# Kernel tuning notes

Hardware: AMD Instinct MI355X
Metric: run time of the kernel (lower is better)

Reference implementation:

```python
import jax, jax.numpy as jnp
import numpy as np

NBUS = 33
B33 = [(1,2),(2,3),(3,4),(4,5),(5,6),(6,7),(7,8),(8,9),(9,10),(10,11),(11,12),(12,13),(13,14),(14,15),(15,16),(16,17),(17,18),(2,19),(19,20),(20,21),(21,22),(3,23),(23,24),(24,25),(6,26),(26,27),(27,28),(28,29),(29,30),(30,31),(31,32),(32,33)]


def setup_inputs() -> dict:
    key = jax.random.key(0)
    k1, k2, k3 = jax.random.split(key, 3)
    B, W, M, F = 32, 128, 100, 8
    N, H, GH, K = NBUS, 256, 128, 3
    rng = np.random.default_rng(0)
    br = np.array(B33) - 1
    src = np.concatenate([br[:, 0], br[:, 1]])
    dst = np.concatenate([br[:, 1], br[:, 0]])
    w_half = rng.uniform(0.5, 2.0, size=br.shape[0]).astype(np.float32)
    p = lambda *s: jnp.asarray(rng.normal(0.0, 0.02, size=s).astype(np.float32))
    z = lambda *s: jnp.zeros(s, jnp.float32)
    return {
        'r_seq': jax.random.normal(k1, (B, W, M), jnp.float32),
        'feat_seq': jax.random.normal(k2, (B, W, F), jnp.float32),
        'x_wls_seq': jax.random.normal(k3, (B, W, 2 * N), jnp.float32),
        'edge_index': jnp.asarray(np.stack([src, dst]).astype(np.int32)),
        'edge_weight': jnp.asarray(np.concatenate([w_half, w_half])),
        'pre_w': p(F + 2, GH), 'pre_b': z(GH),
        'tag_w1': p(K + 1, GH, GH), 'tag_b1': z(GH),
        'tag_w2': p(K + 1, GH, GH), 'tag_b2': z(GH),
        'post_w': p(GH, H), 'post_b': z(H),
        'tp_w1': p(M + 2 * N, H), 'tp_b1': z(H),
        'tp_w2': p(H, H), 'tp_b2': z(H),
        'gru_wih0': p(H, 3 * H), 'gru_whh0': p(H, 3 * H), 'gru_bih0': z(3 * H), 'gru_bhh0': z(3 * H),
        'gru_wih1': p(H, 3 * H), 'gru_whh1': p(H, 3 * H), 'gru_bih1': z(3 * H), 'gru_bhh1': z(3 * H),
        'fg_w': p(H, H), 'fg_b': z(H),
        'fs_w': p(H, H), 'fs_b': z(H),
        'gate_w': p(2 * H, H), 'gate_b': z(H),
        'd1_w': p(H, H), 'd1_b': z(H),
        'd2_w': p(H, 2), 'd2_b': z(2),
    }


def _gru_layer(x, wih, whh, bih, bhh):
    # x: (B, W, Din); torch GRU gate order [r, z, n]
    def step(h, xt):
        gi = xt @ wih + bih
        gh = h @ whh + bhh
        ir, iz, inn = jnp.split(gi, 3, axis=-1)
        hr, hz, hn = jnp.split(gh, 3, axis=-1)
        r = jax.nn.sigmoid(ir + hr)
        zt = jax.nn.sigmoid(iz + hz)
        n = jnp.tanh(inn + r * hn)
        h = (1.0 - zt) * n + zt * h
        return h, h
    h0 = jnp.zeros((x.shape[0], whh.shape[0]), x.dtype)
    _, ys = jax.lax.scan(step, h0, jnp.swapaxes(x, 0, 1))
    return jnp.swapaxes(ys, 0, 1)


def _forward(r_seq, feat_seq, x_wls_seq, edge_index, edge_weight,
             pre_w, pre_b, tag_w1, tag_b1, tag_w2, tag_b2, post_w, post_b,
             tp_w1, tp_b1, tp_w2, tp_b2,
             gru_wih0, gru_whh0, gru_bih0, gru_bhh0,
             gru_wih1, gru_whh1, gru_bih1, gru_bhh1,
             fg_w, fg_b, fs_w, fs_b, gate_w, gate_b,
             d1_w, d1_b, d2_w, d2_b):
    B, W, M = r_seq.shape
    N = NBUS
    # ---- spatial branch (batched TAGConv, K=3, 2 layers) ----
    va = x_wls_seq[..., :N, None]
    vm = x_wls_seq[..., N:, None]
    x_nodes = jnp.concatenate([va, vm], axis=-1)                 # (B,W,N,2)
    feat_n = jnp.broadcast_to(feat_seq[:, :, None, :], (B, W, N, feat_seq.shape[-1]))
    gin = jnp.concatenate([feat_n, x_nodes], axis=-1) @ pre_w + pre_b  # (B,W,N,GH)
    g = gin.reshape(B * W, N, gin.shape[-1])
    src, dst = edge_index[0], edge_index[1]
    # gcn_norm (no self-loops), shared across all B*W graph copies
    deg = jnp.zeros((N,), g.dtype).at[dst].add(edge_weight)
    dinv = jnp.where(deg > 0, deg ** -0.5, 0.0)
    norm = dinv[src] * edge_weight * dinv[dst]                   # (E,)

    def prop(h):  # out[i] = sum_{j->i} norm * h[j], batched over graphs
        return jnp.zeros_like(h).at[:, dst].add(h[:, src] * norm[None, :, None])

    def tag(h, Wk, b):  # TAGConv: sum_k A^k h @ W_k + b
        out = h @ Wk[0]
        hk = h
        for k in range(1, Wk.shape[0]):
            hk = prop(hk)
            out = out + hk @ Wk[k]
        return out + b

    g = jax.nn.relu(tag(g, tag_w1, tag_b1))
    g = tag(g, tag_w2, tag_b2)
    g = g.reshape(B, W, N, -1) @ post_w + post_b                 # (B,W,N,H)
    # ---- temporal branch (MLP -> 2-layer GRU); E_time=None skips MHA ----
    s = jnp.concatenate([r_seq, x_wls_seq], axis=-1)
    s = jax.nn.relu(s @ tp_w1 + tp_b1)
    s = jax.nn.relu(s @ tp_w2 + tp_b2)
    s = _gru_layer(s, gru_wih0, gru_whh0, gru_bih0, gru_bhh0)
    s = _gru_layer(s, gru_wih1, gru_whh1, gru_bih1, gru_bhh1)    # (B,W,H)
    # ---- gated fusion + decoder ----
    g_t = g @ fg_w + fg_b                                        # (B,W,N,H)
    s_t = (s @ fs_w + fs_b)[:, :, None, :]                       # (B,W,1,H)
    s_full = jnp.broadcast_to(s_t, g_t.shape)
    alpha = jax.nn.sigmoid(jnp.concatenate([g_t, s_full], axis=-1) @ gate_w + gate_b)
    u = alpha * g_t + (1.0 - alpha) * s_full
    u = jax.nn.relu(u @ d1_w + d1_b) @ d2_w + d2_b               # (B,W,N,2)
    dx = jnp.concatenate([u[..., 0], u[..., 1]], axis=-1)        # (B,W,2N)
    return x_wls_seq + dx


def reference(r_seq, feat_seq, x_wls_seq, edge_index, edge_weight,
              pre_w, pre_b, tag_w1, tag_b1, tag_w2, tag_b2, post_w, post_b,
              tp_w1, tp_b1, tp_w2, tp_b2,
              gru_wih0, gru_whh0, gru_bih0, gru_bhh0,
              gru_wih1, gru_whh1, gru_bih1, gru_bhh1,
              fg_w, fg_b, fs_w, fs_b, gate_w, gate_b,
              d1_w, d1_b, d2_w, d2_b):
    return _forward(r_seq, feat_seq, x_wls_seq, edge_index, edge_weight,
                    pre_w, pre_b, tag_w1, tag_b1, tag_w2, tag_b2, post_w, post_b,
                    tp_w1, tp_b1, tp_w2, tp_b2,
                    gru_wih0, gru_whh0, gru_bih0, gru_bhh0,
                    gru_wih1, gru_whh1, gru_bih1, gru_bhh1,
                    fg_w, fg_b, fs_w, fs_b, gate_w, gate_b,
                    d1_w, d1_b, d2_w, d2_b)
```

## Files before the change

### kernel.cpp

```cpp
#include <hip/hip_runtime.h>
#include <hip/hip_fp16.h>
#include <cmath>

#define DEV __device__ __forceinline__

typedef unsigned short ushortT;
typedef short bs8 __attribute__((ext_vector_type(8)));
typedef float f32x4 __attribute__((ext_vector_type(4)));
typedef _Float16 f16x2 __attribute__((ext_vector_type(2)));

constexpr int kBW = 4096;
constexpr int kM = 100, kF = 8, kN = 33, kH = 256, kGH = 128, kE = 64;

constexpr int OFF_ROWPTR  = 0;
constexpr int OFF_COLSRC  = 64;
constexpr int OFF_COLNORM = 128;
constexpr int OFF_C       = 192;
constexpr int OFF_WC      = 512;
constexpr int OFF_SPRE    = 33280;
constexpr int OFF_GI      = OFF_SPRE + kBW * kH;
constexpr int OFF_SFUSE   = OFF_GI + kBW * 3 * kH;
constexpr int OFF_SGATE   = OFF_SFUSE + kBW * kH;
constexpr int OFF_WQ0     = OFF_SFUSE;
constexpr int OFF_WQ1     = OFF_SFUSE + 98304;
constexpr int WB_TW1  = 0;
constexpr int WB_TW2  = 65536;
constexpr int WB_WC   = 131072;
constexpr int WB_GATE = 163840;
constexpr int WB_D1   = 229376;
constexpr int WB_TOT  = 294912;

DEV float frcp(float x) { return __builtin_amdgcn_rcpf(x); }
DEV float fsig(float x) { return frcp(1.0f + __expf(-x)); }
DEV float ftanh(float x) { float e = __expf(2.0f * x); return 1.0f - 2.0f * frcp(e + 1.0f); }

DEV ushortT f2bf(float x) {
  unsigned u = __float_as_uint(x);
  unsigned r = u + 0x7fffu + ((u >> 16) & 1u);
  return (ushortT)(r >> 16);
}
DEV float bf2f(ushortT u) { return __uint_as_float(((unsigned)u) << 16); }

DEV f32x4 mfma16(bs8 a, bs8 b, f32x4 c) {
  return __builtin_amdgcn_mfma_f32_16x16x32_bf16(a, b, c, 0, 0, 0);
}
DEV bs8 ldb(const ushortT* p) { return *reinterpret_cast<const bs8*>(p); }

#if __has_builtin(__builtin_amdgcn_fdot2)
DEV float dot2(unsigned w, unsigned hp, float acc) {
  f16x2 wv = __builtin_bit_cast(f16x2, w);
  f16x2 hv = __builtin_bit_cast(f16x2, hp);
  return __builtin_amdgcn_fdot2(wv, hv, acc, false);
}
#else
DEV float dot2(unsigned w, unsigned hp, float acc) {
  f16x2 wv = __builtin_bit_cast(f16x2, w);
  f16x2 hv = __builtin_bit_cast(f16x2, hp);
  acc = fmaf((float)wv.x, (float)hv.x, acc);
  acc = fmaf((float)wv.y, (float)hv.y, acc);
  return acc;
}
#endif

__global__ void k_prep(const int* __restrict__ ei, const float* __restrict__ ew,
                       float* __restrict__ ws) {
  if (blockIdx.x != 0 || threadIdx.x != 0) return;
  int* rowptr = (int*)(ws + OFF_ROWPTR);
  int* colsrc = (int*)(ws + OFF_COLSRC);
  float* colnorm = ws + OFF_COLNORM;
  const int* src = ei;
  const int* dst = ei + kE;
  float deg[kN]; int cnt[kN];
  for (int n = 0; n < kN; ++n) { deg[n] = 0.f; cnt[n] = 0; }
  for (int e = 0; e < kE; ++e) { deg[dst[e]] += ew[e]; cnt[dst[e]]++; }
  float dinv[kN];
  for (int n = 0; n < kN; ++n) dinv[n] = deg[n] > 0.f ? 1.0f / sqrtf(deg[n]) : 0.f;
  int pos[kN];
  int run = 0;
  for (int n = 0; n < kN; ++n) { rowptr[n] = run; pos[n] = run; run += cnt[n]; }
  rowptr[kN] = run;
  for (int e = 0; e < kE; ++e) {
    int d = dst[e];
    int p = pos[d]++;
    colsrc[p] = src[e];
    colnorm[p] = dinv[src[e]] * ew[e] * dinv[d];
  }
}

__global__ void k_wcfold(const float* __restrict__ post_w, const float* __restrict__ post_b,
                         const float* __restrict__ fg_w, const float* __restrict__ fg_b,
                         float* __restrict__ ws) {
  const int j = threadIdx.x;
  if ((int)blockIdx.x < kGH) {
    const int k = blockIdx.x;
    float a = 0.f;
    #pragma unroll 4
    for (int m = 0; m < kH; ++m) a = fmaf(post_w[k * kH + m], fg_w[m * kH + j], a);
    ws[OFF_WC + k * kH + j] = a;
  } else {
    float a = fg_b[j];
    #pragma unroll 4
    for (int m = 0; m < kH; ++m) a = fmaf(post_b[m], fg_w[m * kH + j], a);
    ws[OFF_C + j] = a;
  }
}

__global__ void k_wq(const float* __restrict__ w0, const float* __restrict__ w1,
                     float* __restrict__ ws) {
  const int idx = blockIdx.x * 256 + threadIdx.x;
  if (idx >= 2 * 98304) return;
  const int layer = idx / 98304;
  const int rem = idx - layer * 98304;
  const int p = rem / 768, j = rem - p * 768;
  const float* w = layer ? w1 : w0;
  unsigned* dst = (unsigned*)(ws + (layer ? OFF_WQ1 : OFF_WQ0));
  __half2 v = __floats2half2_rn(w[(2 * p) * 768 + j], w[(2 * p + 1) * 768 + j]);
  dst[rem] = *reinterpret_cast<unsigned*>(&v);
}

__global__ void k_wprep(const float* __restrict__ tw1, const float* __restrict__ tw2,
                        const float* __restrict__ gatew, const float* __restrict__ d1w,
                        float* __restrict__ ws) {
  const int idx = blockIdx.x * 256 + threadIdx.x;
  if (idx >= WB_TOT) return;
  ushortT* WB = (ushortT*)(ws + OFF_GI);
  float v; int dst;
  if (idx < 65536) {
    int s = idx >> 14, r = idx & 16383, k = r >> 7, col = r & 127;
    v = tw1[(s << 14) + (k << 7) + col]; dst = WB_TW1 + (s << 14) + (col << 7) + k;
  } else if (idx < 131072) {
    int i = idx - 65536; int s = i >> 14, r = i & 16383, k = r >> 7, col = r & 127;
    v = tw2[(s << 14) + (k << 7) + col]; dst = WB_TW2 + (s << 14) + (col << 7) + k;
  } else if (idx < 163840) {
    int i = idx - 131072; int k = i & 127, col = i >> 7;
    v = ws[OFF_WC + (k << 8) + col]; dst = WB_WC + (col << 7) + k;
  } else if (idx < 229376) {
    int i = idx - 163840; int k = i & 255, col = i >> 8;
    v = gatew[(k << 8) + col]; dst = WB_GATE + (col << 8) + k;
  } else {
    int i = idx - 229376; int k = i & 255, col = i >> 8;
    v = d1w[(k << 8) + col]; dst = WB_D1 + (col << 8) + k;
  }
  WB[dst] = f2bf(v);
}

__global__ __launch_bounds__(256) void k_tpmlp(
    const float* __restrict__ r_seq, const float* __restrict__ x_wls,
    const float* __restrict__ w1, const float* __restrict__ b1,
    const float* __restrict__ w2, const float* __restrict__ b2,
    float* __restrict__ sout) {
  __shared__ float inr[16][kM + 2 * kN];
  __shared__ float h1[16][kH];
  const int bw0 = blockIdx.x * 16, tid = threadIdx.x;
  #pragma unroll
  for (int r = 0; r < 16; ++r) {
    for (int c = tid; c < kM + 2 * kN; c += 256)
      inr[r][c] = (c < kM) ? r_seq[(bw0 + r) * kM + c]
                           : x_wls[(bw0 + r) * 2 * kN + (c - kM)];
  }
  __syncthreads();
  float acc[16];
  {
    const float bb = b1[tid];
    #pragma unroll
    for (int r = 0; r < 16; ++r) acc[r] = bb;
  }
  for (int k = 0; k < kM + 2 * kN; ++k) {
    const float w = w1[k * kH + tid];
    #pragma unroll
    for (int r = 0; r < 16; ++r) acc[r] = fmaf(inr[r][k], w, acc[r]);
  }
  #pragma unroll
  for (int r = 0; r < 16; ++r) h1[r][tid] = fmaxf(acc[r], 0.f);
  __syncthreads();
  {
    const float bb = b2[tid];
    #pragma unroll
    for (int r = 0; r < 16; ++r) acc[r] = bb;
  }
  #pragma unroll 2
  for (int k = 0; k < kH; ++k) {
    const float w = w2[k * kH + tid];
    #pragma unroll
    for (int r = 0; r < 16; ++r) acc[r] = fmaf(h1[r][k], w, acc[r]);
  }
  #pragma unroll
  for (int r = 0; r < 16; ++r) sout[(bw0 + r) * kH + tid] = fmaxf(acc[r], 0.f);
}

__global__ __launch_bounds__(768) void k_gigemm(
    const float* __restrict__ sin, const float* __restrict__ wih,
    const float* __restrict__ bih, float* __restrict__ gi) {
  __shared__ float sr[16][kH];
  const int bw0 = blockIdx.x * 16, tid = threadIdx.x;
  for (int i = tid; i < 16 * kH; i += 768) sr[i >> 8][i & 255] = sin[bw0 * kH + i];
  __syncthreads();
  float acc[16];
  {
    const float bb = bih[tid];
    #pragma unroll
    for (int r = 0; r < 16; ++r) acc[r] = bb;
  }
  #pragma unroll 2
  for (int k = 0; k < kH; ++k) {
    const float w = wih[k * 768 + tid];
    #pragma unroll
    for (int r = 0; r < 16; ++r) acc[r] = fmaf(sr[r][k], w, acc[r]);
  }
  #pragma unroll
  for (int r = 0; r < 16; ++r) gi[(bw0 + r) * 768 + tid] = acc[r];
}

__global__ __launch_bounds__(768, 3) void k_scan(
    const float* __restrict__ gi, const float* __restrict__ wq,
    const float* __restrict__ bhh, float* __restrict__ sout) {
  __shared__ float h[kH];
  __shared__ __align__(16) unsigned hpk[kH / 2];
  __shared__ float gh[3 * kH];
  const int b = blockIdx.x, tid = threadIdx.x;
  const unsigned* wqp = (const unsigned*)wq;
  unsigned wr[128];
  #pragma unroll
  for (int p = 0; p < 128; ++p) wr[p] = wqp[p * 768 + tid];
  if (tid < kH) h[tid] = 0.f;
  if (tid < kH / 2) hpk[tid] = 0u;
  __syncthreads();
  const float bb = bhh[tid];
  for (int t = 0; t < 128; ++t) {
    const float* girow = gi + (b * 128 + t) * 768;
    float a0 = bb, a1 = 0.f, a2 = 0.f, a3 = 0.f;
    #pragma unroll
    for (int q = 0; q < 32; ++q) {
      const uint4 hp = *reinterpret_cast<const uint4*>(hpk + 4 * q);
      a0 = dot2(wr[4 * q + 0], hp.x, a0);
      a1 = dot2(wr[4 * q + 1], hp.y, a1);
      a2 = dot2(wr[4 * q + 2], hp.z, a2);
      a3 = dot2(wr[4 * q + 3], hp.w, a3);
    }
    gh[tid] = (a0 + a1) + (a2 + a3);
    __syncthreads();
    if (tid < kH) {
      float r = fsig(girow[tid] + gh[tid]);
      float z = fsig(girow[kH + tid] + gh[kH + tid]);
      float n = ftanh(fmaf(r, gh[2 * kH + tid], girow[2 * kH + tid]));
      float hn = (1.f - z) * n + z * h[tid];
      h[tid] = hn;
      reinterpret_cast<__half*>(hpk)[tid] = __float2half(hn);
      sout[(b * 128 + t) * kH + tid] = hn;
    }
    __syncthreads();
  }
}

__global__ __launch_bounds__(256) void k_fsgate(
    const float* __restrict__ s1, const float* __restrict__ fsw,
    const float* __restrict__ fsb, const float* __restrict__ gw,
    const float* __restrict__ gb, float* __restrict__ sfuse,
    float* __restrict__ sgate) {
  __shared__ float sr[16][kH], sf[16][kH];
  const int bw0 = blockIdx.x * 16, tid = threadIdx.x;
  for (int i = tid; i < 16 * kH; i += 256) sr[i >> 8][i & 255] = s1[bw0 * kH + i];
  __syncthreads();
  float acc[16];
  {
    const float bb = fsb[tid];
    #pragma unroll
    for (int r = 0; r < 16; ++r) acc[r] = bb;
  }
  #pragma unroll 2
  for (int k = 0; k < kH; ++k) {
    const float w = fsw[k * kH + tid];
    #pragma unroll
    for (int r = 0; r < 16; ++r) acc[r] = fmaf(sr[r][k], w, acc[r]);
  }
  #pragma unroll
  for (int r = 0; r < 16; ++r) { sf[r][tid] = acc[r]; sfuse[(bw0 + r) * kH + tid] = acc[r]; }
  __syncthreads();
  {
    const float bb = gb[tid];
    #pragma unroll
    for (int r = 0; r < 16; ++r) acc[r] = bb;
  }
  #pragma unroll 2
  for (int k = 0; k < kH; ++k) {
    const float w = gw[(kH + k) * kH + tid];
    #pragma unroll
    for (int r = 0; r < 16; ++r) acc[r] = fmaf(sf[r][k], w, acc[r]);
  }
  #pragma unroll
  for (int r = 0; r < 16; ++r) sgate[(bw0 + r) * kH + tid] = acc[r];
}


constexpr int SB0 = 0;
constexpr int SB1 = 36 * 136;
constexpr int S_TOT = 2 * 36 * 136;

DEV void propb(ushortT* __restrict__ dst, const ushortT* __restrict__ src,
               const int* __restrict__ rp, const int* __restrict__ cs,
               const float* __restrict__ cn) {
  for (int idx = threadIdx.x; idx < kN * 64; idx += 256) {
    const int n = idx >> 6, j2 = idx & 63;
    float a0 = 0.f, a1 = 0.f;
    const int p1 = rp[n + 1];
    for (int p = rp[n]; p < p1; ++p) {
      const unsigned v = *(const unsigned*)(src + cs[p] * 136 + 2 * j2);
      const float w = cn[p];
      a0 = fmaf(__uint_as_float(v << 16), w, a0);
      a1 = fmaf(__uint_as_float(v & 0xffff0000u), w, a1);
    }
    *(unsigned*)(dst + n * 136 + 2 * j2) = (unsigned)f2bf(a0) | ((unsigned)f2bf(a1) << 16);
  }
}

template <bool RELU>
DEV void tag_mfma(ushortT* __restrict__ Sb, const ushortT* __restrict__ WT,
                  const float* __restrict__ b, const int* __restrict__ rp,
                  const int* __restrict__ cs, const float* __restrict__ cn,
                  int wv, int lane) {
  const int lr = lane & 15, lg = lane >> 4;
  f32x4 acc[6];
  #pragma unroll
  for (int i = 0; i < 6; ++i) acc[i] = (f32x4){0.f, 0.f, 0.f, 0.f};
  ushortT* bufs[2] = {Sb + SB0, Sb + SB1};
  int cur = 0;
  #pragma unroll
  for (int s = 0; s < 4; ++s) {
    const ushortT* A = bufs[cur];
    #pragma unroll
    for (int ks = 0; ks < 4; ++ks) {
      const int kof = ks * 32 + lg * 8;
      bs8 a0 = ldb(A + (lr) * 136 + kof);
      bs8 a1 = ldb(A + (16 + lr) * 136 + kof);
      bs8 a2 = ldb(A + (32 + lr) * 136 + kof);
      #pragma unroll
      for (int nt = 0; nt < 2; ++nt) {
        const int col = (wv * 2 + nt) * 16 + lr;
        bs8 bb = ldb(WT + (s << 14) + (col << 7) + kof);
        acc[0 + nt] = mfma16(a0, bb, acc[0 + nt]);
        acc[2 + nt] = mfma16(a1, bb, acc[2 + nt]);
        acc[4 + nt] = mfma16(a2, bb, acc[4 + nt]);
      }
    }
    if (s < 3) {
      propb(bufs[cur ^ 1], bufs[cur], rp, cs, cn);
      __syncthreads();
      cur ^= 1;
    }
  }
  __syncthreads();
  #pragma unroll
  for (int mt = 0; mt < 3; ++mt)
    #pragma unroll
    for (int nt = 0; nt < 2; ++nt) {
      const int col = (wv * 2 + nt) * 16 + lr;
      const float bias = b[col];
      const f32x4 v = acc[mt * 2 + nt];
      #pragma unroll
      for (int r = 0; r < 4; ++r) {
        const int row = mt * 16 + lg * 4 + r;
        if (row < kN) {
          float x = v[r] + bias;
          if (RELU) x = fmaxf(x, 0.f);
          (Sb + SB0)[row * 136 + col] = f2bf(x);
        }
      }
    }
  __syncthreads();
}

__global__ __launch_bounds__(256, 4) void k_fused(
    const float* __restrict__ feat_seq, const float* __restrict__ x_wls,
    const float* __restrict__ pre_w, const float* __restrict__ pre_b,
    const float* __restrict__ tb1, const float* __restrict__ tb2,
    const float* __restrict__ d1b, const float* __restrict__ d2w,
    const float* __restrict__ d2b, const float* __restrict__ ws,
    const float* __restrict__ sfuse, const float* __restrict__ sgate,
    float* __restrict__ out) {
  __shared__ __align__(16) ushortT S[S_TOT];
  __shared__ float sfrow[kH], sgrow[kH];
  __shared__ float xw[2 * kN];
  __shared__ float featl[kF];
  __shared__ int rp[kN + 1], cs[kE];
  __shared__ float cn[kE];
  __shared__ float part[4][48][2];
  const int tid = threadIdx.x, bw = blockIdx.x;
  const int wv = tid >> 6, lane = tid & 63;
  const int lr = lane & 15, lg = lane >> 4;
  const ushortT* WB = (const ushortT*)(ws + OFF_GI);
  ushortT* GT = S;

  sfrow[tid] = sfuse[bw * kH + tid];
  sgrow[tid] = sgate[bw * kH + tid];
  if (tid < 2 * kN) xw[tid] = x_wls[bw * 2 * kN + tid];
  else if (tid >= 66 && tid < 66 + kF) featl[tid - 66] = feat_seq[bw * kF + (tid - 66)];
  if (tid >= 128 && tid < 128 + kN + 1) rp[tid - 128] = ((const int*)(ws + OFF_ROWPTR))[tid - 128];
  if (tid >= 192) {
    cs[tid - 192] = ((const int*)(ws + OFF_COLSRC))[tid - 192];
    cn[tid - 192] = ws[OFF_COLNORM + (tid - 192)];
  }
  for (int i = tid; i < 3 * kGH; i += 256) {
    S[SB0 + kN * 136 + i] = 0;
    S[SB1 + kN * 136 + i] = 0;
  }
  __syncthreads();

  for (int idx = tid; idx < kN * kGH; idx += 256) {
    const int n = idx >> 7, j = idx & 127;
    float a = pre_b[j];
    #pragma unroll
    for (int f = 0; f < kF; ++f) a = fmaf(featl[f], pre_w[f * kGH + j], a);
    a = fmaf(xw[n], pre_w[8 * kGH + j], a);
    a = fmaf(xw[kN + n], pre_w[9 * kGH + j], a);
    S[SB0 + n * 136 + j] = f2bf(a);
  }
  __syncthreads();

  tag_mfma<true >(S, WB + WB_TW1, tb1, rp, cs, cn, wv, lane);
  tag_mfma<false>(S, WB + WB_TW2, tb2, rp, cs, cn, wv, lane);

  {
    f32x4 acc[12];
    #pragma unroll
    for (int i = 0; i < 12; ++i) acc[i] = (f32x4){0.f, 0.f, 0.f, 0.f};
    #pragma unroll
    for (int ks = 0; ks < 4; ++ks) {
      const int kof = ks * 32 + lg * 8;
      bs8 a0 = ldb(S + SB0 + (lr) * 136 + kof);
      bs8 a1 = ldb(S + SB0 + (16 + lr) * 136 + kof);
      bs8 a2 = ldb(S + SB0 + (32 + lr) * 136 + kof);
      #pragma unroll
      for (int nt = 0; nt < 4; ++nt) {
        const int col = (wv * 4 + nt) * 16 + lr;
        bs8 bb = ldb(WB + WB_WC + (col << 7) + kof);
        acc[0 + nt] = mfma16(a0, bb, acc[0 + nt]);
        acc[4 + nt] = mfma16(a1, bb, acc[4 + nt]);
        acc[8 + nt] = mfma16(a2, bb, acc[8 + nt]);
      }
    }
    __syncthreads();
    #pragma unroll
    for (int mt = 0; mt < 3; ++mt)
      #pragma unroll
      for (int nt = 0; nt < 4; ++nt) {
        const int col = (wv * 4 + nt) * 16 + lr;
        const float cb = ws[OFF_C + col];
        const f32x4 v = acc[mt * 4 + nt];
        #pragma unroll
        for (int r = 0; r < 4; ++r) {
          const int row = mt * 16 + lg * 4 + r;
          if (row < kN) GT[row * 264 + col] = f2bf(v[r] + cb);
        }
      }
    __syncthreads();
  }

  {
    f32x4 acc[12];
    #pragma unroll
    for (int i = 0; i < 12; ++i) acc[i] = (f32x4){0.f, 0.f, 0.f, 0.f};
    #pragma unroll 2
    for (int ks = 0; ks < 8; ++ks) {
      const int kof = ks * 32 + lg * 8;
      const int r2 = (32 + lr) < 36 ? (32 + lr) : 35;
      bs8 a0 = ldb(GT + (lr) * 264 + kof);
      bs8 a1 = ldb(GT + (16 + lr) * 264 + kof);
      bs8 a2 = ldb(GT + r2 * 264 + kof);
      #pragma unroll
      for (int nt = 0; nt < 4; ++nt) {
        const int col = (wv * 4 + nt) * 16 + lr;
        bs8 bb = ldb(WB + WB_GATE + (col << 8) + kof);
        acc[0 + nt] = mfma16(a0, bb, acc[0 + nt]);
        acc[4 + nt] = mfma16(a1, bb, acc[4 + nt]);
        acc[8 + nt] = mfma16(a2, bb, acc[8 + nt]);
      }
    }
    #pragma unroll
    for (int mt = 0; mt < 3; ++mt)
      #pragma unroll
      for (int nt = 0; nt < 4; ++nt) {
        const int col = (wv * 4 + nt) * 16 + lr;
        const float sg = sgrow[col], sf = sfrow[col];
        #pragma unroll
        for (int r = 0; r < 4; ++r) {
          const int row = mt * 16 + lg * 4 + r;
          if (row < kN) {
            const float al = fsig(acc[mt * 4 + nt][r] + sg);
            const float gt = bf2f(GT[row * 264 + col]);
            acc[mt * 4 + nt][r] = al * gt + (1.f - al) * sf;
          }
        }
      }
    __syncthreads();
    #pragma unroll
    for (int mt = 0; mt < 3; ++mt)
      #pragma unroll
      for (int nt = 0; nt < 4; ++nt) {
        const int col = (wv * 4 + nt) * 16 + lr;
        #pragma unroll
        for (int r = 0; r < 4; ++r) {
          const int row = mt * 16 + lg * 4 + r;
          if (row < kN) GT[row * 264 + col] = f2bf(acc[mt * 4 + nt][r]);
        }
      }
    __syncthreads();
  }

  {
    f32x4 acc[12];
    #pragma unroll
    for (int i = 0; i < 12; ++i) acc[i] = (f32x4){0.f, 0.f, 0.f, 0.f};
    #pragma unroll 2
    for (int ks = 0; ks < 8; ++ks) {
      const int kof = ks * 32 + lg * 8;
      const int r2 = (32 + lr) < 36 ? (32 + lr) : 35;
      bs8 a0 = ldb(GT + (lr) * 264 + kof);
      bs8 a1 = ldb(GT + (16 + lr) * 264 + kof);
      bs8 a2 = ldb(GT + r2 * 264 + kof);
      #pragma unroll
      for (int nt = 0; nt < 4; ++nt) {
        const int col = (wv * 4 + nt) * 16 + lr;
        bs8 bb = ldb(WB + WB_D1 + (col << 8) + kof);
        acc[0 + nt] = mfma16(a0, bb, acc[0 + nt]);
        acc[4 + nt] = mfma16(a1, bb, acc[4 + nt]);
        acc[8 + nt] = mfma16(a2, bb, acc[8 + nt]);
      }
    }
    float p0[3][4], p1[3][4];
    #pragma unroll
    for (int mt = 0; mt < 3; ++mt)
      #pragma unroll
      for (int r = 0; r < 4; ++r) { p0[mt][r] = 0.f; p1[mt][r] = 0.f; }
    #pragma unroll
    for (int nt = 0; nt < 4; ++nt) {
      const int col = (wv * 4 + nt) * 16 + lr;
      const float db = d1b[col];
      const float2 dp = *reinterpret_cast<const float2*>(d2w + col * 2);
      #pragma unroll
      for (int mt = 0; mt < 3; ++mt)
        #pragma unroll
        for (int r = 0; r < 4; ++r) {
          const float v = fmaxf(acc[mt * 4 + nt][r] + db, 0.f);
          p0[mt][r] = fmaf(v, dp.x, p0[mt][r]);
          p1[mt][r] = fmaf(v, dp.y, p1[mt][r]);
        }
    }
    #pragma unroll
    for (int mt = 0; mt < 3; ++mt)
      #pragma unroll
      for (int r = 0; r < 4; ++r) {
        #pragma unroll
        for (int off = 1; off < 16; off <<= 1) {
          p0[mt][r] += __shfl_xor(p0[mt][r], off, 64);
          p1[mt][r] += __shfl_xor(p1[mt][r], off, 64);
        }
      }
    if (lr == 0) {
      #pragma unroll
      for (int mt = 0; mt < 3; ++mt)
        #pragma unroll
        for (int r = 0; r < 4; ++r) {
          const int row = mt * 16 + lg * 4 + r;
          part[wv][row][0] = p0[mt][r];
          part[wv][row][1] = p1[mt][r];
        }
    }
    __syncthreads();
    if (tid < 66) {
      const int c = tid >= 33 ? 1 : 0;
      const int n = tid - 33 * c;
      float s = d2b[c];
      #pragma unroll
      for (int w = 0; w < 4; ++w) s += part[w][n][c];
      out[bw * 66 + tid] = xw[tid] + s;
    }
  }
}

extern "C" void kernel_launch(void* const* d_in, const int* in_sizes, int n_in,
                              void* d_out, int out_size, void* d_ws, size_t ws_size,
                              hipStream_t stream) {
  const float* r_seq  = (const float*)d_in[0];
  const float* feat   = (const float*)d_in[1];
  const float* x_wls  = (const float*)d_in[2];
  const int*   eidx   = (const int*)d_in[3];
  const float* ew     = (const float*)d_in[4];
  const float* pre_w  = (const float*)d_in[5];
  const float* pre_b  = (const float*)d_in[6];
  const float* tag_w1 = (const float*)d_in[7];
  const float* tag_b1 = (const float*)d_in[8];
  const float* tag_w2 = (const float*)d_in[9];
  const float* tag_b2 = (const float*)d_in[10];
  const float* post_w = (const float*)d_in[11];
  const float* post_b = (const float*)d_in[12];
  const float* tp_w1  = (const float*)d_in[13];
  const float* tp_b1  = (const float*)d_in[14];
  const float* tp_w2  = (const float*)d_in[15];
  const float* tp_b2  = (const float*)d_in[16];
  const float* wih0   = (const float*)d_in[17];
  const float* whh0   = (const float*)d_in[18];
  const float* bih0   = (const float*)d_in[19];
  const float* bhh0   = (const float*)d_in[20];
  const float* wih1   = (const float*)d_in[21];
  const float* whh1   = (const float*)d_in[22];
  const float* bih1   = (const float*)d_in[23];
  const float* bhh1   = (const float*)d_in[24];
  const float* fg_w   = (const float*)d_in[25];
  const float* fg_b   = (const float*)d_in[26];
  const float* fs_w   = (const float*)d_in[27];
  const float* fs_b   = (const float*)d_in[28];
  const float* gate_w = (const float*)d_in[29];
  const float* gate_b = (const float*)d_in[30];
  const float* d1_w   = (const float*)d_in[31];
  const float* d1_b   = (const float*)d_in[32];
  const float* d2_w   = (const float*)d_in[33];
  const float* d2_b   = (const float*)d_in[34];
  float* ws = (float*)d_ws;
  float* outp = (float*)d_out;

  k_prep<<<1, 64, 0, stream>>>(eidx, ew, ws);
  k_wcfold<<<kGH + 1, kH, 0, stream>>>(post_w, post_b, fg_w, fg_b, ws);
  k_wq<<<768, 256, 0, stream>>>(whh0, whh1, ws);
  k_tpmlp<<<kBW / 16, 256, 0, stream>>>(r_seq, x_wls, tp_w1, tp_b1, tp_w2, tp_b2,
                                        ws + OFF_SPRE);
  k_gigemm<<<kBW / 16, 768, 0, stream>>>(ws + OFF_SPRE, wih0, bih0, ws + OFF_GI);
  k_scan<<<32, 768, 0, stream>>>(ws + OFF_GI, ws + OFF_WQ0, bhh0, ws + OFF_SPRE);
  k_gigemm<<<kBW / 16, 768, 0, stream>>>(ws + OFF_SPRE, wih1, bih1, ws + OFF_GI);
  k_scan<<<32, 768, 0, stream>>>(ws + OFF_GI, ws + OFF_WQ1, bhh1, ws + OFF_SPRE);
  k_wprep<<<(WB_TOT + 255) / 256, 256, 0, stream>>>(tag_w1, tag_w2, gate_w, d1_w, ws);
  k_fsgate<<<kBW / 16, 256, 0, stream>>>(ws + OFF_SPRE, fs_w, fs_b, gate_w, gate_b,
                                         ws + OFF_SFUSE, ws + OFF_SGATE);
  k_fused<<<kBW, 256, 0, stream>>>(feat, x_wls, pre_w, pre_b, tag_b1, tag_b2,
                                   d1_b, d2_w, d2_b, ws, ws + OFF_SFUSE,
                                   ws + OFF_SGATE, outp);
}
```

Before: 1.068 ms.

## Double k_fused block to 512 threads, halving per-wave column tiles

The fused per-window kernel now launches 8 waves instead of 4, and each wave owns half as many output column tiles in the TAG, fold, gate and decoder MFMA stages. Strided loops for propagation, pre-projection and zero-fill step by 512, and the decoder partial-sum reduction grows to 8 wave slots. The goal is more latency hiding and fewer accumulator registers per wave. In exchange, each wave re-reads the shared A tiles for a smaller N slice, and the larger block may limit how many blocks fit per CU.

```diff
diff --git a/kernel.cpp b/kernel.cpp
--- a/kernel.cpp
+++ b/kernel.cpp
@@ -299,7 +299,7 @@
 DEV void propb(ushortT* __restrict__ dst, const ushortT* __restrict__ src,
                const int* __restrict__ rp, const int* __restrict__ cs,
                const float* __restrict__ cn) {
-  for (int idx = threadIdx.x; idx < kN * 64; idx += 256) {
+  for (int idx = threadIdx.x; idx < kN * 64; idx += 512) {
     const int n = idx >> 6, j2 = idx & 63;
     float a0 = 0.f, a1 = 0.f;
     const int p1 = rp[n + 1];
@@ -319,57 +319,47 @@
                   const int* __restrict__ cs, const float* __restrict__ cn,
                   int wv, int lane) {
   const int lr = lane & 15, lg = lane >> 4;
-  f32x4 acc[6];
-  #pragma unroll
-  for (int i = 0; i < 6; ++i) acc[i] = (f32x4){0.f, 0.f, 0.f, 0.f};
-  ushortT* bufs[2] = {Sb + SB0, Sb + SB1};
-  int cur = 0;
+  const int col = wv * 16 + lr;
+  f32x4 acc[3];
+  #pragma unroll
+  for (int i = 0; i < 3; ++i) acc[i] = (f32x4){0.f, 0.f, 0.f, 0.f};
   #pragma unroll
   for (int s = 0; s < 4; ++s) {
-    const ushortT* A = bufs[cur];
+    const ushortT* A = Sb + ((s & 1) ? SB1 : SB0);
+    ushortT* Bn      = Sb + ((s & 1) ? SB0 : SB1);
     #pragma unroll
     for (int ks = 0; ks < 4; ++ks) {
       const int kof = ks * 32 + lg * 8;
       bs8 a0 = ldb(A + (lr) * 136 + kof);
       bs8 a1 = ldb(A + (16 + lr) * 136 + kof);
       bs8 a2 = ldb(A + (32 + lr) * 136 + kof);
-      #pragma unroll
-      for (int nt = 0; nt < 2; ++nt) {
-        const int col = (wv * 2 + nt) * 16 + lr;
-        bs8 bb = ldb(WT + (s << 14) + (col << 7) + kof);
-        acc[0 + nt] = mfma16(a0, bb, acc[0 + nt]);
-        acc[2 + nt] = mfma16(a1, bb, acc[2 + nt]);
-        acc[4 + nt] = mfma16(a2, bb, acc[4 + nt]);
-      }
+      bs8 bb = ldb(WT + (s << 14) + (col << 7) + kof);
+      acc[0] = mfma16(a0, bb, acc[0]);
+      acc[1] = mfma16(a1, bb, acc[1]);
+      acc[2] = mfma16(a2, bb, acc[2]);
     }
     if (s < 3) {
-      propb(bufs[cur ^ 1], bufs[cur], rp, cs, cn);
+      propb(Bn, A, rp, cs, cn);
       __syncthreads();
-      cur ^= 1;
-    }
-  }
-  __syncthreads();
+    }
+  }
+  __syncthreads();
+  const float bias = b[col];
   #pragma unroll
   for (int mt = 0; mt < 3; ++mt)
     #pragma unroll
-    for (int nt = 0; nt < 2; ++nt) {
-      const int col = (wv * 2 + nt) * 16 + lr;
-      const float bias = b[col];
-      const f32x4 v = acc[mt * 2 + nt];
-      #pragma unroll
-      for (int r = 0; r < 4; ++r) {
-        const int row = mt * 16 + lg * 4 + r;
-        if (row < kN) {
-          float x = v[r] + bias;
-          if (RELU) x = fmaxf(x, 0.f);
-          (Sb + SB0)[row * 136 + col] = f2bf(x);
-        }
-      }
-    }
-  __syncthreads();
-}
-
-__global__ __launch_bounds__(256, 4) void k_fused(
+    for (int r = 0; r < 4; ++r) {
+      const int row = mt * 16 + lg * 4 + r;
+      if (row < kN) {
+        float x = acc[mt][r] + bias;
+        if (RELU) x = fmaxf(x, 0.f);
+        (Sb + SB0)[row * 136 + col] = f2bf(x);
+      }
+    }
+  __syncthreads();
+}
+
+__global__ __launch_bounds__(512, 4) void k_fused(
     const float* __restrict__ feat_seq, const float* __restrict__ x_wls,
     const float* __restrict__ pre_w, const float* __restrict__ pre_b,
     const float* __restrict__ tb1, const float* __restrict__ tb2,
@@ -383,29 +373,29 @@
   __shared__ float featl[kF];
   __shared__ int rp[kN + 1], cs[kE];
   __shared__ float cn[kE];
-  __shared__ float part[4][48][2];
+  __shared__ float part[8][48][2];
   const int tid = threadIdx.x, bw = blockIdx.x;
   const int wv = tid >> 6, lane = tid & 63;
   const int lr = lane & 15, lg = lane >> 4;
   const ushortT* WB = (const ushortT*)(ws + OFF_GI);
   ushortT* GT = S;
 
-  sfrow[tid] = sfuse[bw * kH + tid];
-  sgrow[tid] = sgate[bw * kH + tid];
+  if (tid < kH) sfrow[tid] = sfuse[bw * kH + tid];
+  else if (tid < 2 * kH) sgrow[tid - kH] = sgate[bw * kH + (tid - kH)];
   if (tid < 2 * kN) xw[tid] = x_wls[bw * 2 * kN + tid];
   else if (tid >= 66 && tid < 66 + kF) featl[tid - 66] = feat_seq[bw * kF + (tid - 66)];
   if (tid >= 128 && tid < 128 + kN + 1) rp[tid - 128] = ((const int*)(ws + OFF_ROWPTR))[tid - 128];
-  if (tid >= 192) {
+  if (tid >= 192 && tid < 256) {
     cs[tid - 192] = ((const int*)(ws + OFF_COLSRC))[tid - 192];
     cn[tid - 192] = ws[OFF_COLNORM + (tid - 192)];
   }
-  for (int i = tid; i < 3 * kGH; i += 256) {
+  for (int i = tid; i < 3 * 136; i += 512) {
     S[SB0 + kN * 136 + i] = 0;
     S[SB1 + kN * 136 + i] = 0;
   }
   __syncthreads();
 
-  for (int idx = tid; idx < kN * kGH; idx += 256) {
+  for (int idx = tid; idx < kN * kGH; idx += 512) {
     const int n = idx >> 7, j = idx & 127;
     float a = pre_b[j];
     #pragma unroll
@@ -420,9 +410,9 @@
   tag_mfma<false>(S, WB + WB_TW2, tb2, rp, cs, cn, wv, lane);
 
   {
-    f32x4 acc[12];
-    #pragma unroll
-    for (int i = 0; i < 12; ++i) acc[i] = (f32x4){0.f, 0.f, 0.f, 0.f};
+    f32x4 acc[6];
+    #pragma unroll
+    for (int i = 0; i < 6; ++i) acc[i] = (f32x4){0.f, 0.f, 0.f, 0.f};
     #pragma unroll
     for (int ks = 0; ks < 4; ++ks) {
       const int kof = ks * 32 + lg * 8;
@@ -430,22 +420,22 @@
       bs8 a1 = ldb(S + SB0 + (16 + lr) * 136 + kof);
       bs8 a2 = ldb(S + SB0 + (32 + lr) * 136 + kof);
       #pragma unroll
-      for (int nt = 0; nt < 4; ++nt) {
-        const int col = (wv * 4 + nt) * 16 + lr;
+      for (int nt = 0; nt < 2; ++nt) {
+        const int col = (wv * 2 + nt) * 16 + lr;
         bs8 bb = ldb(WB + WB_WC + (col << 7) + kof);
         acc[0 + nt] = mfma16(a0, bb, acc[0 + nt]);
-        acc[4 + nt] = mfma16(a1, bb, acc[4 + nt]);
-        acc[8 + nt] = mfma16(a2, bb, acc[8 + nt]);
+        acc[2 + nt] = mfma16(a1, bb, acc[2 + nt]);
+        acc[4 + nt] = mfma16(a2, bb, acc[4 + nt]);
       }
     }
     __syncthreads();
     #pragma unroll
     for (int mt = 0; mt < 3; ++mt)
       #pragma unroll
-      for (int nt = 0; nt < 4; ++nt) {
-        const int col = (wv * 4 + nt) * 16 + lr;
+      for (int nt = 0; nt < 2; ++nt) {
+        const int col = (wv * 2 + nt) * 16 + lr;
         const float cb = ws[OFF_C + col];
-        const f32x4 v = acc[mt * 4 + nt];
+        const f32x4 v = acc[mt * 2 + nt];
         #pragma unroll
         for (int r = 0; r < 4; ++r) {
           const int row = mt * 16 + lg * 4 + r;
@@ -456,9 +446,9 @@
   }
 
   {
-    f32x4 acc[12];
-    #pragma unroll
-    for (int i = 0; i < 12; ++i) acc[i] = (f32x4){0.f, 0.f, 0.f, 0.f};
+    f32x4 acc[6];
+    #pragma unroll
+    for (int i = 0; i < 6; ++i) acc[i] = (f32x4){0.f, 0.f, 0.f, 0.f};
     #pragma unroll 2
     for (int ks = 0; ks < 8; ++ks) {
       const int kof = ks * 32 + lg * 8;
@@ -467,27 +457,27 @@
       bs8 a1 = ldb(GT + (16 + lr) * 264 + kof);
       bs8 a2 = ldb(GT + r2 * 264 + kof);
       #pragma unroll
-      for (int nt = 0; nt < 4; ++nt) {
-        const int col = (wv * 4 + nt) * 16 + lr;
+      for (int nt = 0; nt < 2; ++nt) {
+        const int col = (wv * 2 + nt) * 16 + lr;
         bs8 bb = ldb(WB + WB_GATE + (col << 8) + kof);
         acc[0 + nt] = mfma16(a0, bb, acc[0 + nt]);
-        acc[4 + nt] = mfma16(a1, bb, acc[4 + nt]);
-        acc[8 + nt] = mfma16(a2, bb, acc[8 + nt]);
+        acc[2 + nt] = mfma16(a1, bb, acc[2 + nt]);
+        acc[4 + nt] = mfma16(a2, bb, acc[4 + nt]);
       }
     }
     #pragma unroll
     for (int mt = 0; mt < 3; ++mt)
       #pragma unroll
-      for (int nt = 0; nt < 4; ++nt) {
-        const int col = (wv * 4 + nt) * 16 + lr;
+      for (int nt = 0; nt < 2; ++nt) {
+        const int col = (wv * 2 + nt) * 16 + lr;
         const float sg = sgrow[col], sf = sfrow[col];
         #pragma unroll
         for (int r = 0; r < 4; ++r) {
           const int row = mt * 16 + lg * 4 + r;
           if (row < kN) {
-            const float al = fsig(acc[mt * 4 + nt][r] + sg);
+            const float al = fsig(acc[mt * 2 + nt][r] + sg);
             const float gt = bf2f(GT[row * 264 + col]);
-            acc[mt * 4 + nt][r] = al * gt + (1.f - al) * sf;
+            acc[mt * 2 + nt][r] = al * gt + (1.f - al) * sf;
           }
         }
       }
@@ -495,21 +485,21 @@
     #pragma unroll
     for (int mt = 0; mt < 3; ++mt)
       #pragma unroll
-      for (int nt = 0; nt < 4; ++nt) {
-        const int col = (wv * 4 + nt) * 16 + lr;
+      for (int nt = 0; nt < 2; ++nt) {
+        const int col = (wv * 2 + nt) * 16 + lr;
         #pragma unroll
         for (int r = 0; r < 4; ++r) {
           const int row = mt * 16 + lg * 4 + r;
-          if (row < kN) GT[row * 264 + col] = f2bf(acc[mt * 4 + nt][r]);
+          if (row < kN) GT[row * 264 + col] = f2bf(acc[mt * 2 + nt][r]);
         }
       }
     __syncthreads();
   }
 
   {
-    f32x4 acc[12];
-    #pragma unroll
-    for (int i = 0; i < 12; ++i) acc[i] = (f32x4){0.f, 0.f, 0.f, 0.f};
+    f32x4 acc[6];
+    #pragma unroll
+    for (int i = 0; i < 6; ++i) acc[i] = (f32x4){0.f, 0.f, 0.f, 0.f};
     #pragma unroll 2
     for (int ks = 0; ks < 8; ++ks) {
       const int kof = ks * 32 + lg * 8;
@@ -518,12 +508,12 @@
       bs8 a1 = ldb(GT + (16 + lr) * 264 + kof);
       bs8 a2 = ldb(GT + r2 * 264 + kof);
       #pragma unroll
-      for (int nt = 0; nt < 4; ++nt) {
-        const int col = (wv * 4 + nt) * 16 + lr;
+      for (int nt = 0; nt < 2; ++nt) {
+        const int col = (wv * 2 + nt) * 16 + lr;
         bs8 bb = ldb(WB + WB_D1 + (col << 8) + kof);
         acc[0 + nt] = mfma16(a0, bb, acc[0 + nt]);
-        acc[4 + nt] = mfma16(a1, bb, acc[4 + nt]);
-        acc[8 + nt] = mfma16(a2, bb, acc[8 + nt]);
+        acc[2 + nt] = mfma16(a1, bb, acc[2 + nt]);
+        acc[4 + nt] = mfma16(a2, bb, acc[4 + nt]);
       }
     }
     float p0[3][4], p1[3][4];
@@ -532,15 +522,15 @@
       #pragma unroll
       for (int r = 0; r < 4; ++r) { p0[mt][r] = 0.f; p1[mt][r] = 0.f; }
     #pragma unroll
-    for (int nt = 0; nt < 4; ++nt) {
-      const int col = (wv * 4 + nt) * 16 + lr;
+    for (int nt = 0; nt < 2; ++nt) {
+      const int col = (wv * 2 + nt) * 16 + lr;
       const float db = d1b[col];
       const float2 dp = *reinterpret_cast<const float2*>(d2w + col * 2);
       #pragma unroll
       for (int mt = 0; mt < 3; ++mt)
         #pragma unroll
         for (int r = 0; r < 4; ++r) {
-          const float v = fmaxf(acc[mt * 4 + nt][r] + db, 0.f);
+          const float v = fmaxf(acc[mt * 2 + nt][r] + db, 0.f);
           p0[mt][r] = fmaf(v, dp.x, p0[mt][r]);
           p1[mt][r] = fmaf(v, dp.y, p1[mt][r]);
         }
@@ -571,7 +561,7 @@
       const int n = tid - 33 * c;
       float s = d2b[c];
       #pragma unroll
-      for (int w = 0; w < 4; ++w) s += part[w][n][c];
+      for (int w = 0; w < 8; ++w) s += part[w][n][c];
       out[bw * 66 + tid] = xw[tid] + s;
     }
   }
@@ -630,7 +620,7 @@
   k_wprep<<<(WB_TOT + 255) / 256, 256, 0, stream>>>(tag_w1, tag_w2, gate_w, d1_w, ws);
   k_fsgate<<<kBW / 16, 256, 0, stream>>>(ws + OFF_SPRE, fs_w, fs_b, gate_w, gate_b,
                                          ws + OFF_SFUSE, ws + OFF_SGATE);
-  k_fused<<<kBW, 256, 0, stream>>>(feat, x_wls, pre_w, pre_b, tag_b1, tag_b2,
+  k_fused<<<kBW, 512, 0, stream>>>(feat, x_wls, pre_w, pre_b, tag_b1, tag_b2,
                                    d1_b, d2_w, d2_b, ws, ws + OFF_SFUSE,
                                    ws + OFF_SGATE, outp);
 }
```

Measured after the change: 1.030 ms. -3.6%, faster.
